# Kernel tuning notes

Measured on AMD Instinct MI355X. Metric: run time of the kernel, lower is better.

## Reference

```python
import jax, jax.numpy as jnp
import numpy as np


def setup_inputs() -> dict:
    key = jax.random.key(0)
    k1, k2, k3 = jax.random.split(key, 3)
    B, H, N, D = 4, 16, 4096, 128
    return {
        "q": jax.random.normal(k1, (B, H, N, D), dtype=jnp.float32),
        "k": jax.random.normal(k2, (B, H, N, D), dtype=jnp.float32),
        "v": jax.random.normal(k3, (B, H, N, D), dtype=jnp.float32),
    }


def reference(q, k, v):
    # Aaren-style numerically stable online-softmax linear-attention scan.
    # q, k, v: [B, H, N, D]
    scale = 1.0
    B, H, N, D = q.shape
    qs = jnp.moveaxis(q * scale, 2, 0)  # [N, B, H, D] time-major
    ks = jnp.moveaxis(k, 2, 0)
    vs = jnp.moveaxis(v, 2, 0)

    n0 = jnp.zeros((B, H, D), dtype=q.dtype)
    d0 = jnp.zeros((B, H, 1), dtype=q.dtype)
    m0 = jnp.full((B, H, 1), -jnp.inf, dtype=q.dtype)

    def step(carry, inp):
        n_p, d_p, m_p = carry
        q_t, k_t, v_t = inp
        alpha = jnp.sum(q_t * k_t, axis=-1, keepdims=True)  # [B, H, 1]
        m_t = jnp.maximum(m_p, alpha)
        exp_mdiff = jnp.exp(m_p - m_t)
        exp_adiff = jnp.exp(alpha - m_t)
        d_t = exp_mdiff * d_p + exp_adiff
        n_t = exp_mdiff * n_p + exp_adiff * v_t
        y_t = n_t / d_t
        return (n_t, d_t, m_t), y_t

    _, y = jax.lax.scan(step, (n0, d0, m0), (qs, ks, vs))  # y: [N, B, H, D]
    return jnp.moveaxis(y, 0, 2)  # [B, H, N, D]
```

## Files before the change

kernel.cpp:

```cpp
#include <hip/hip_runtime.h>
#include <math.h>
#include <stdint.h>

static constexpr int ROWS = 64;
static constexpr int NSEQ = 4096;
static constexpr int DIM  = 128;
static constexpr int SC   = 16;
static constexpr int SPR  = NSEQ / SC;
static constexpr int NSC  = ROWS * SPR;
static constexpr int VC   = 64;
static constexpr int VPR  = NSEQ / VC;
static constexpr int NVC  = ROWS * VPR;
static constexpr int SPC  = VC / SC;

typedef __attribute__((address_space(3))) uint32_t  lds_u32;
typedef const __attribute__((address_space(1))) uint32_t g_u32;

__global__ __launch_bounds__(128) void k_alpha(
    const float* __restrict__ q, const float* __restrict__ k,
    float* __restrict__ alpha, float* __restrict__ cM, float* __restrict__ cD)
{
    __shared__ float lds[8192];
    const int l    = threadIdx.x & 63;
    const int w    = threadIdx.x >> 6;
    const int tile = blockIdx.x;
    const int b4   = tile * (32 * DIM);

    #pragma unroll
    for (int i = 0; i < 8; ++i) {
        const int p  = w * 8192 + i * 1024 + l * 16;
        const int ps = p ^ (((p >> 9) & 7) << 4);
        __builtin_amdgcn_global_load_lds((g_u32*)(q + b4 + (ps >> 2)),
                                         (lds_u32*)&lds[(w * 8192 + i * 1024) >> 2],
                                         16, 0, 0);
    }
    #pragma unroll
    for (int i = 0; i < 8; ++i) {
        const int p  = w * 8192 + i * 1024 + l * 16;
        const int ps = p ^ (((p >> 9) & 7) << 4);
        __builtin_amdgcn_global_load_lds((g_u32*)(k + b4 + (ps >> 2)),
                                         (lds_u32*)&lds[4096 + ((w * 8192 + i * 1024) >> 2)],
                                         16, 0, 0);
    }
    asm volatile("s_waitcnt vmcnt(0)" ::: "memory");
    __syncthreads();

    const int tl = w * 16 + (l >> 2);
    const int c  = l & 3;
    const int sw = (tl & 7) << 4;
    float acc = 0.f;
    #pragma unroll
    for (int j = 0; j < 8; ++j) {
        const int off = tl * 512 + ((c * 128 + j * 16) ^ sw);
        const float4 qv = *(const float4*)((const char*)lds + off);
        const float4 kv = *(const float4*)((const char*)lds + 16384 + off);
        acc += qv.x * kv.x + qv.y * kv.y + qv.z * kv.z + qv.w * kv.w;
    }
    acc += __shfl_xor(acc, 1);
    acc += __shfl_xor(acc, 2);

    float M = acc;
    #pragma unroll
    for (int m = 4; m <= 32; m <<= 1) M = fmaxf(M, __shfl_xor(M, m));
    float e = (c == 0) ? __expf(acc - M) : 0.f;
    #pragma unroll
    for (int m = 4; m <= 32; m <<= 1) e += __shfl_xor(e, m);

    if (c == 0) alpha[tile * 32 + tl] = acc;
    if (l == 0) { cM[tile * 2 + w] = M; cD[tile * 2 + w] = e; }
}

__global__ __launch_bounds__(256) void k_scan(
    const float* __restrict__ alpha, const float* __restrict__ cM,
    const float* __restrict__ cD,
    float* __restrict__ pM, float* __restrict__ pD, float2* __restrict__ coefCW)
{
    __shared__ float lM[SPR], lD[SPR], lpM[SPR];
    const int row = blockIdx.x;
    const int tid = threadIdx.x;

    lM[tid] = cM[row * SPR + tid];
    lD[tid] = cD[row * SPR + tid];
    __syncthreads();

    if (tid == 0) {
        float m = -INFINITY, d = 0.f;
        for (int sl = 0; sl < SPR; ++sl) {
            lpM[sl] = m;
            pM[row * SPR + sl] = m; pD[row * SPR + sl] = d;
            const float M = lM[sl], D = lD[sl];
            const float mn = fmaxf(m, M);
            d = d * __expf(m - mn) + D * __expf(M - mn);
            m = mn;
        }
    }
    __syncthreads();

    const int li = tid & 15, grp = tid >> 4;
    for (int sl = grp; sl < SPR; sl += 16) {
        const int s = row * SPR + sl;
        const float a = alpha[s * SC + li];
        float m = a;
        #pragma unroll
        for (int d = 1; d < 16; d <<= 1) {
            const float o = __shfl_up(m, d, 16);
            if (li >= d) m = fmaxf(m, o);
        }
        const float carry = lpM[sl];
        const float mf = fmaxf(m, carry);
        float mp = __shfl_up(mf, 1, 16);
        if (li == 0) mp = carry;
        const float cc = __expf(mp - mf);
        const float wt = __expf(a - mf);
        coefCW[s * SC + li] = make_float2(cc, wt);
    }
}

__global__ __launch_bounds__(256) void k_agg(
    const float* __restrict__ v, const float2* __restrict__ coefCW,
    float2* __restrict__ aggN)
{
    const int lane  = threadIdx.x & 63;
    const int C     = blockIdx.x * 4 + (threadIdx.x >> 6);
    const int vbase = C * (VC * DIM);
    const int cbase = __builtin_amdgcn_readfirstlane(C * VC);

    float nx = 0.f, ny = 0.f;
    for (int t0 = 0; t0 < VC; t0 += 8) {
        float2 cw[8], vv[8];
        #pragma unroll
        for (int u = 0; u < 8; ++u) cw[u] = coefCW[cbase + t0 + u];
        #pragma unroll
        for (int u = 0; u < 8; ++u)
            vv[u] = *((const float2*)(v + vbase + (t0 + u) * DIM) + lane);
        #pragma unroll
        for (int u = 0; u < 8; ++u) {
            nx = cw[u].x * nx + cw[u].y * vv[u].x;
            ny = cw[u].x * ny + cw[u].y * vv[u].y;
        }
    }
    aggN[C * (DIM / 2) + lane] = make_float2(nx, ny);
}

__global__ __launch_bounds__(128) void k_pref(
    float* __restrict__ aggN, const float* __restrict__ pM)
{
    const int row = blockIdx.x;
    const int d   = threadIdx.x;
    float state = 0.f;
    for (int C0 = 0; C0 < VPR; C0 += 8) {
        float nb[8], f1[8];
        #pragma unroll
        for (int u = 0; u < 8; ++u) {
            const int C  = C0 + u;
            const int Cg = row * VPR + C;
            nb[u] = aggN[Cg * DIM + d];
            const bool last = (C == VPR - 1);
            const float mp  = pM[SPC * Cg];
            const float mp2 = last ? 0.f : pM[SPC * Cg + SPC];
            f1[u] = last ? 0.f : __expf(mp - mp2);
        }
        #pragma unroll
        for (int u = 0; u < 8; ++u) {
            const float nc = nb[u];
            aggN[(row * VPR + C0 + u) * DIM + d] = state;
            state = state * f1[u] + nc;
        }
    }
}

__global__ __launch_bounds__(256) void k_out(
    const float* __restrict__ v, const float2* __restrict__ coefCW,
    const float2* __restrict__ preN, const float* __restrict__ pD,
    float* __restrict__ y)
{
    const int lane  = threadIdx.x & 63;
    const int C     = blockIdx.x * 4 + (threadIdx.x >> 6);
    const int vbase = C * (VC * DIM);
    const int cbase = __builtin_amdgcn_readfirstlane(C * VC);

    float2 n  = preN[C * (DIM / 2) + lane];
    float dch = pD[SPC * C];

    for (int t0 = 0; t0 < VC; t0 += 8) {
        float2 cw[8], vv[8];
        #pragma unroll
        for (int u = 0; u < 8; ++u) cw[u] = coefCW[cbase + t0 + u];
        #pragma unroll
        for (int u = 0; u < 8; ++u)
            vv[u] = *((const float2*)(v + vbase + (t0 + u) * DIM) + lane);
        #pragma unroll
        for (int u = 0; u < 8; ++u) {
            n.x = cw[u].x * n.x + cw[u].y * vv[u].x;
            n.y = cw[u].x * n.y + cw[u].y * vv[u].y;
            dch = cw[u].x * dch + cw[u].y;
            const float rd = __builtin_amdgcn_rcpf(dch);
            *((float2*)(y + vbase + (t0 + u) * DIM) + lane) =
                make_float2(n.x * rd, n.y * rd);
        }
    }
}

extern "C" void kernel_launch(void* const* d_in, const int* in_sizes, int n_in,
                              void* d_out, int out_size, void* d_ws, size_t ws_size,
                              hipStream_t stream) {
    const float* q = (const float*)d_in[0];
    const float* k = (const float*)d_in[1];
    const float* v = (const float*)d_in[2];
    float* y  = (float*)d_out;
    float* ws = (float*)d_ws;

    float*  coefCWf = ws;
    float*  pM      = coefCWf + 2 * ROWS * NSEQ;
    float*  pD      = pM + NSC;
    float*  cM      = pD + NSC;
    float*  cD      = cM + NSC;
    float*  U       = cD + NSC;
    float*  alphaA  = U;
    float*  aggNf   = U;
    float2* coefCW  = (float2*)coefCWf;
    float2* aggN2   = (float2*)aggNf;

    k_alpha<<<ROWS * NSEQ / 32, 128, 0, stream>>>(q, k, alphaA, cM, cD);
    k_scan<<<ROWS, 256, 0, stream>>>(alphaA, cM, cD, pM, pD, coefCW);
    k_agg<<<NVC / 4, 256, 0, stream>>>(v, coefCW, aggN2);
    k_pref<<<ROWS, DIM, 0, stream>>>(aggNf, pM);
    k_out<<<NVC / 4, 256, 0, stream>>>(v, coefCW, aggN2, pD, y);
}
```

Measured before the change: 159.6 us.

## Double-buffer q/k tiles in k_alpha and halve scan chunk size

k_alpha now has each 256-thread block process 8 consecutive 32-token tiles. The next tile's q and k are prefetched into a second LDS buffer via global_load_lds while the current tile's dot products and per-chunk max/sum are computed, so load latency overlaps compute and fewer blocks are launched. The per-wave chunk shrinks from 16 to 8 tokens, so k_scan is updated to 8-lane segmented scans and loads twice as many chunk summaries. The risk is that the single-thread serial carry loop in k_scan now walks 512 chunks per row instead of 256, which adds latency to that step.

```diff
diff --git a/kernel.cpp b/kernel.cpp
--- a/kernel.cpp
+++ b/kernel.cpp
@@ -5,7 +5,7 @@
 static constexpr int ROWS = 64;
 static constexpr int NSEQ = 4096;
 static constexpr int DIM  = 128;
-static constexpr int SC   = 16;
+static constexpr int SC   = 8;
 static constexpr int SPR  = NSEQ / SC;
 static constexpr int NSC  = ROWS * SPR;
 static constexpr int VC   = 64;
@@ -16,58 +16,91 @@
 typedef __attribute__((address_space(3))) uint32_t  lds_u32;
 typedef const __attribute__((address_space(1))) uint32_t g_u32;
 
-__global__ __launch_bounds__(128) void k_alpha(
+__global__ __launch_bounds__(256) void k_alpha(
     const float* __restrict__ q, const float* __restrict__ k,
     float* __restrict__ alpha, float* __restrict__ cM, float* __restrict__ cD)
 {
-    __shared__ float lds[8192];
-    const int l    = threadIdx.x & 63;
-    const int w    = threadIdx.x >> 6;
-    const int tile = blockIdx.x;
-    const int b4   = tile * (32 * DIM);
-
+    __shared__ float lds[2][8192];
+    const int tid   = threadIdx.x;
+    const int l     = tid & 63;
+    const int w     = tid >> 6;
+    const int c     = l & 7;
+    const int t     = w * 8 + (l >> 3);
+    const int sw    = (t & 7) << 4;
+    const int first = blockIdx.x * 8;
+
+    int psrc[4];
     #pragma unroll
-    for (int i = 0; i < 8; ++i) {
-        const int p  = w * 8192 + i * 1024 + l * 16;
-        const int ps = p ^ (((p >> 9) & 7) << 4);
-        __builtin_amdgcn_global_load_lds((g_u32*)(q + b4 + (ps >> 2)),
-                                         (lds_u32*)&lds[(w * 8192 + i * 1024) >> 2],
-                                         16, 0, 0);
-    }
-    #pragma unroll
-    for (int i = 0; i < 8; ++i) {
-        const int p  = w * 8192 + i * 1024 + l * 16;
-        const int ps = p ^ (((p >> 9) & 7) << 4);
-        __builtin_amdgcn_global_load_lds((g_u32*)(k + b4 + (ps >> 2)),
-                                         (lds_u32*)&lds[4096 + ((w * 8192 + i * 1024) >> 2)],
-                                         16, 0, 0);
-    }
-    asm volatile("s_waitcnt vmcnt(0)" ::: "memory");
-    __syncthreads();
-
-    const int tl = w * 16 + (l >> 2);
-    const int c  = l & 3;
-    const int sw = (tl & 7) << 4;
-    float acc = 0.f;
+    for (int i = 0; i < 4; ++i) {
+        const int p = w * 4096 + i * 1024 + l * 16;
+        psrc[i] = (p ^ (((p >> 9) & 7) << 4)) >> 2;
+    }
+
+    float aA[8], sM[8], sD[8];
+
+    #define STAGE(BUF, TILE)                                                   \
+        do {                                                                   \
+            const float* qb_ = q + (size_t)(TILE) * 4096;                      \
+            const float* kb_ = k + (size_t)(TILE) * 4096;                      \
+            _Pragma("unroll")                                                  \
+            for (int i = 0; i < 4; ++i)                                        \
+                __builtin_amdgcn_global_load_lds((g_u32*)(qb_ + psrc[i]),      \
+                    (lds_u32*)&lds[BUF][(w * 4096 + i * 1024) >> 2], 16, 0, 0);\
+            _Pragma("unroll")                                                  \
+            for (int i = 0; i < 4; ++i)                                        \
+                __builtin_amdgcn_global_load_lds((g_u32*)(kb_ + psrc[i]),      \
+                    (lds_u32*)&lds[BUF][4096 + ((w * 4096 + i * 1024) >> 2)],  \
+                    16, 0, 0);                                                 \
+        } while (0)
+
+    STAGE(0, first);
+
     #pragma unroll
     for (int j = 0; j < 8; ++j) {
-        const int off = tl * 512 + ((c * 128 + j * 16) ^ sw);
-        const float4 qv = *(const float4*)((const char*)lds + off);
-        const float4 kv = *(const float4*)((const char*)lds + 16384 + off);
-        acc += qv.x * kv.x + qv.y * kv.y + qv.z * kv.z + qv.w * kv.w;
-    }
-    acc += __shfl_xor(acc, 1);
-    acc += __shfl_xor(acc, 2);
-
-    float M = acc;
+        const int buf = j & 1;
+        if (j < 7) {
+            STAGE(buf ^ 1, first + j + 1);
+            asm volatile("s_waitcnt vmcnt(8)" ::: "memory");
+        } else {
+            asm volatile("s_waitcnt vmcnt(0)" ::: "memory");
+        }
+        __builtin_amdgcn_s_barrier();
+        __builtin_amdgcn_sched_barrier(0);
+
+        float acc = 0.f;
+        #pragma unroll
+        for (int jj = 0; jj < 4; ++jj) {
+            const int off = t * 512 + (((c << 6) | (jj << 4)) ^ sw);
+            const float4 qv = *(const float4*)((const char*)&lds[buf][0] + off);
+            const float4 kv = *(const float4*)((const char*)&lds[buf][0] + 16384 + off);
+            acc += qv.x * kv.x + qv.y * kv.y + qv.z * kv.z + qv.w * kv.w;
+        }
+        acc += __shfl_xor(acc, 1);
+        acc += __shfl_xor(acc, 2);
+        acc += __shfl_xor(acc, 4);
+
+        float M = acc;
+        M = fmaxf(M, __shfl_xor(M, 8));
+        M = fmaxf(M, __shfl_xor(M, 16));
+        M = fmaxf(M, __shfl_xor(M, 32));
+        float e = (c == 0) ? __expf(acc - M) : 0.f;
+        e += __shfl_xor(e, 8);
+        e += __shfl_xor(e, 16);
+        e += __shfl_xor(e, 32);
+
+        aA[j] = acc; sM[j] = M; sD[j] = e;
+
+        __builtin_amdgcn_sched_barrier(0);
+        __builtin_amdgcn_s_barrier();
+    }
+    #undef STAGE
+
     #pragma unroll
-    for (int m = 4; m <= 32; m <<= 1) M = fmaxf(M, __shfl_xor(M, m));
-    float e = (c == 0) ? __expf(acc - M) : 0.f;
-    #pragma unroll
-    for (int m = 4; m <= 32; m <<= 1) e += __shfl_xor(e, m);
-
-    if (c == 0) alpha[tile * 32 + tl] = acc;
-    if (l == 0) { cM[tile * 2 + w] = M; cD[tile * 2 + w] = e; }
+    for (int j = 0; j < 8; ++j) {
+        const int tile = first + j;
+        if (c == 0) alpha[tile * 32 + t] = aA[j];
+        if (l == 0) { cM[tile * 4 + w] = sM[j]; cD[tile * 4 + w] = sD[j]; }
+    }
 }
 
 __global__ __launch_bounds__(256) void k_scan(
@@ -79,8 +112,10 @@
     const int row = blockIdx.x;
     const int tid = threadIdx.x;
 
-    lM[tid] = cM[row * SPR + tid];
-    lD[tid] = cD[row * SPR + tid];
+    lM[tid]       = cM[row * SPR + tid];
+    lM[tid + 256] = cM[row * SPR + tid + 256];
+    lD[tid]       = cD[row * SPR + tid];
+    lD[tid + 256] = cD[row * SPR + tid + 256];
     __syncthreads();
 
     if (tid == 0) {
@@ -96,19 +131,19 @@
     }
     __syncthreads();
 
-    const int li = tid & 15, grp = tid >> 4;
-    for (int sl = grp; sl < SPR; sl += 16) {
+    const int li = tid & 7, grp = tid >> 3;
+    for (int sl = grp; sl < SPR; sl += 32) {
         const int s = row * SPR + sl;
         const float a = alpha[s * SC + li];
         float m = a;
         #pragma unroll
-        for (int d = 1; d < 16; d <<= 1) {
-            const float o = __shfl_up(m, d, 16);
+        for (int d = 1; d < 8; d <<= 1) {
+            const float o = __shfl_up(m, d, 8);
             if (li >= d) m = fmaxf(m, o);
         }
         const float carry = lpM[sl];
         const float mf = fmaxf(m, carry);
-        float mp = __shfl_up(mf, 1, 16);
+        float mp = __shfl_up(mf, 1, 8);
         if (li == 0) mp = carry;
         const float cc = __expf(mp - mf);
         const float wt = __expf(a - mf);
@@ -221,7 +256,7 @@
     float2* coefCW  = (float2*)coefCWf;
     float2* aggN2   = (float2*)aggNf;
 
-    k_alpha<<<ROWS * NSEQ / 32, 128, 0, stream>>>(q, k, alphaA, cM, cD);
+    k_alpha<<<(ROWS * NSEQ / 32) / 8, 256, 0, stream>>>(q, k, alphaA, cM, cD);
     k_scan<<<ROWS, 256, 0, stream>>>(alphaA, cM, cD, pM, pD, coefCW);
     k_agg<<<NVC / 4, 256, 0, stream>>>(v, coefCW, aggN2);
     k_pref<<<ROWS, DIM, 0, stream>>>(aggNf, pM);
```

Result: slower. 176.0 us (+10.3%).

## Halve scan chunk size and double threads per alpha tile

Applied to the files above, without the earlier changes.

Doubles the k_alpha block to 256 threads. Two waves now load q and two load k into separate LDS buffers, and 8 lanes per row compute each dot product. The statistics chunk size drops from 16 to 8, so each wave emits one chunk max and sum. k_scan is adapted to the doubled chunk count, and SPC changes accordingly for the downstream kernels. The goal is more memory-level parallelism and occupancy in the alpha pass. The cost is that the single-thread serial carry loop in k_scan now runs twice as many iterations.

```diff
diff --git a/kernel.cpp b/kernel.cpp
--- a/kernel.cpp
+++ b/kernel.cpp
@@ -5,7 +5,7 @@
 static constexpr int ROWS = 64;
 static constexpr int NSEQ = 4096;
 static constexpr int DIM  = 128;
-static constexpr int SC   = 16;
+static constexpr int SC   = 8;
 static constexpr int SPR  = NSEQ / SC;
 static constexpr int NSC  = ROWS * SPR;
 static constexpr int VC   = 64;
@@ -16,58 +16,66 @@
 typedef __attribute__((address_space(3))) uint32_t  lds_u32;
 typedef const __attribute__((address_space(1))) uint32_t g_u32;
 
-__global__ __launch_bounds__(128) void k_alpha(
+__global__ __launch_bounds__(256) void k_alpha(
     const float* __restrict__ q, const float* __restrict__ k,
     float* __restrict__ alpha, float* __restrict__ cM, float* __restrict__ cD)
 {
-    __shared__ float lds[8192];
-    const int l    = threadIdx.x & 63;
-    const int w    = threadIdx.x >> 6;
+    __shared__ float qs[4096];
+    __shared__ float ks[4096];
+    const int tid  = threadIdx.x;
+    const int l    = tid & 63;
+    const int w    = tid >> 6;
     const int tile = blockIdx.x;
-    const int b4   = tile * (32 * DIM);
-
-    #pragma unroll
-    for (int i = 0; i < 8; ++i) {
-        const int p  = w * 8192 + i * 1024 + l * 16;
-        const int ps = p ^ (((p >> 9) & 7) << 4);
-        __builtin_amdgcn_global_load_lds((g_u32*)(q + b4 + (ps >> 2)),
-                                         (lds_u32*)&lds[(w * 8192 + i * 1024) >> 2],
-                                         16, 0, 0);
-    }
-    #pragma unroll
-    for (int i = 0; i < 8; ++i) {
-        const int p  = w * 8192 + i * 1024 + l * 16;
-        const int ps = p ^ (((p >> 9) & 7) << 4);
-        __builtin_amdgcn_global_load_lds((g_u32*)(k + b4 + (ps >> 2)),
-                                         (lds_u32*)&lds[4096 + ((w * 8192 + i * 1024) >> 2)],
-                                         16, 0, 0);
-    }
-    asm volatile("s_waitcnt vmcnt(0)" ::: "memory");
+    const size_t base = (size_t)tile * (32 * DIM);
+
+    if (w < 2) {
+        #pragma unroll
+        for (int i = 0; i < 8; ++i) {
+            const int p  = w * 8192 + i * 1024 + l * 16;
+            const int ps = p ^ (((p >> 9) & 7) << 4);
+            __builtin_amdgcn_global_load_lds((g_u32*)(q + base + (ps >> 2)),
+                (lds_u32*)&qs[(w * 8192 + i * 1024) >> 2], 16, 0, 0);
+        }
+    } else {
+        #pragma unroll
+        for (int i = 0; i < 8; ++i) {
+            const int p  = (w - 2) * 8192 + i * 1024 + l * 16;
+            const int ps = p ^ (((p >> 9) & 7) << 4);
+            __builtin_amdgcn_global_load_lds((g_u32*)(k + base + (ps >> 2)),
+                (lds_u32*)&ks[((w - 2) * 8192 + i * 1024) >> 2], 16, 0, 0);
+        }
+    }
     __syncthreads();
 
-    const int tl = w * 16 + (l >> 2);
-    const int c  = l & 3;
-    const int sw = (tl & 7) << 4;
+    const int t  = tid >> 3;
+    const int x  = tid & 7;
+    const int sw = (t & 7) << 4;
     float acc = 0.f;
     #pragma unroll
-    for (int j = 0; j < 8; ++j) {
-        const int off = tl * 512 + ((c * 128 + j * 16) ^ sw);
-        const float4 qv = *(const float4*)((const char*)lds + off);
-        const float4 kv = *(const float4*)((const char*)lds + 16384 + off);
+    for (int j = 0; j < 4; ++j) {
+        const int off = t * 512 + ((x * 64 + j * 16) ^ sw);
+        const float4 qv = *(const float4*)((const char*)qs + off);
+        const float4 kv = *(const float4*)((const char*)ks + off);
         acc += qv.x * kv.x + qv.y * kv.y + qv.z * kv.z + qv.w * kv.w;
     }
     acc += __shfl_xor(acc, 1);
     acc += __shfl_xor(acc, 2);
+    acc += __shfl_xor(acc, 4);
 
     float M = acc;
-    #pragma unroll
-    for (int m = 4; m <= 32; m <<= 1) M = fmaxf(M, __shfl_xor(M, m));
-    float e = (c == 0) ? __expf(acc - M) : 0.f;
-    #pragma unroll
-    for (int m = 4; m <= 32; m <<= 1) e += __shfl_xor(e, m);
-
-    if (c == 0) alpha[tile * 32 + tl] = acc;
-    if (l == 0) { cM[tile * 2 + w] = M; cD[tile * 2 + w] = e; }
+    M = fmaxf(M, __shfl_xor(M, 8));
+    M = fmaxf(M, __shfl_xor(M, 16));
+    M = fmaxf(M, __shfl_xor(M, 32));
+    float e = (x == 0) ? __expf(acc - M) : 0.f;
+    e += __shfl_xor(e, 8);
+    e += __shfl_xor(e, 16);
+    e += __shfl_xor(e, 32);
+
+    if (x == 0) alpha[tile * 32 + t] = acc;
+    if (l == 0) {
+        const int s = tile * 4 + w;
+        cM[s] = M; cD[s] = e;
+    }
 }
 
 __global__ __launch_bounds__(256) void k_scan(
@@ -79,8 +87,10 @@
     const int row = blockIdx.x;
     const int tid = threadIdx.x;
 
-    lM[tid] = cM[row * SPR + tid];
-    lD[tid] = cD[row * SPR + tid];
+    lM[tid]       = cM[row * SPR + tid];
+    lM[tid + 256] = cM[row * SPR + tid + 256];
+    lD[tid]       = cD[row * SPR + tid];
+    lD[tid + 256] = cD[row * SPR + tid + 256];
     __syncthreads();
 
     if (tid == 0) {
@@ -96,19 +106,19 @@
     }
     __syncthreads();
 
-    const int li = tid & 15, grp = tid >> 4;
-    for (int sl = grp; sl < SPR; sl += 16) {
+    const int li = tid & 7, grp = tid >> 3;
+    for (int sl = grp; sl < SPR; sl += 32) {
         const int s = row * SPR + sl;
         const float a = alpha[s * SC + li];
         float m = a;
         #pragma unroll
-        for (int d = 1; d < 16; d <<= 1) {
-            const float o = __shfl_up(m, d, 16);
+        for (int d = 1; d < 8; d <<= 1) {
+            const float o = __shfl_up(m, d, 8);
             if (li >= d) m = fmaxf(m, o);
         }
         const float carry = lpM[sl];
         const float mf = fmaxf(m, carry);
-        float mp = __shfl_up(mf, 1, 16);
+        float mp = __shfl_up(mf, 1, 8);
         if (li == 0) mp = carry;
         const float cc = __expf(mp - mf);
         const float wt = __expf(a - mf);
@@ -221,7 +231,7 @@
     float2* coefCW  = (float2*)coefCWf;
     float2* aggN2   = (float2*)aggNf;
 
-    k_alpha<<<ROWS * NSEQ / 32, 128, 0, stream>>>(q, k, alphaA, cM, cD);
+    k_alpha<<<ROWS * NSEQ / 32, 256, 0, stream>>>(q, k, alphaA, cM, cD);
     k_scan<<<ROWS, 256, 0, stream>>>(alphaA, cM, cD, pM, pD, coefCW);
     k_agg<<<NVC / 4, 256, 0, stream>>>(v, coefCW, aggN2);
     k_pref<<<ROWS, DIM, 0, stream>>>(aggNf, pM);
```

Measured after the change: 171.2 us. 7.3% more time.
